# Kernel tuning notes

Hardware: AMD Instinct MI355X
Metric: run time of the kernel (lower is better)

## Reference

```python
import jax, jax.numpy as jnp
import numpy as np

N, E, B = 50000, 100000, 512   # nodes, edges, graphs
H, F_NODE, F_EDGE, T_OUT = 64, 16, 8, 1
T = 3                           # message-passing steps


def setup_inputs() -> dict:
    key = jax.random.key(0)
    ks = jax.random.split(key, 18)

    def w(k, shape, fan_in):
        return jax.random.normal(k, shape, dtype=jnp.float32) / np.sqrt(fan_in)

    return {
        "node_features": jax.random.normal(ks[0], (N, F_NODE), dtype=jnp.float32),
        "edge_features": jax.random.normal(ks[1], (E, F_EDGE), dtype=jnp.float32),
        "Esrc": jax.random.randint(ks[2], (E,), 0, N, dtype=jnp.int32),
        "Etgt": jax.random.randint(ks[3], (E,), 0, N, dtype=jnp.int32),
        "batch": jnp.sort(jax.random.randint(ks[4], (N,), 0, B, dtype=jnp.int32)),
        # input linear: node_features -> hidden
        "Win": w(ks[5], (H, F_NODE), F_NODE),
        "bin_": jnp.zeros((H,), jnp.float32),
        # edge encoder MLP: edge_features -> hidden -> hidden*hidden
        "We1": w(ks[6], (H, F_EDGE), F_EDGE),
        "be1": jnp.zeros((H,), jnp.float32),
        "We2": w(ks[7], (H * H, H), H),
        "be2": jnp.zeros((H * H,), jnp.float32),
        # GRU cell (shared across T steps)
        "Wih": w(ks[8], (3 * H, H), H),
        "bih": jnp.zeros((3 * H,), jnp.float32),
        "Whh": w(ks[9], (3 * H, H), H),
        "bhh": jnp.zeros((3 * H,), jnp.float32),
        # output linear: hidden -> target_features
        "Wout": w(ks[10], (T_OUT, H), H),
        "bout": jnp.zeros((T_OUT,), jnp.float32),
    }


def _gru(x, h, Wih, bih, Whh, bhh):
    gi = x @ Wih.T + bih            # [N, 3H]
    gh = h @ Whh.T + bhh
    i_r, i_z, i_n = jnp.split(gi, 3, axis=-1)
    h_r, h_z, h_n = jnp.split(gh, 3, axis=-1)
    r = jax.nn.sigmoid(i_r + h_r)
    z = jax.nn.sigmoid(i_z + h_z)
    n = jnp.tanh(i_n + r * h_n)
    return (1.0 - z) * n + z * h


def reference(node_features, edge_features, Esrc, Etgt, batch,
              Win, bin_, We1, be1, We2, be2,
              Wih, bih, Whh, bhh, Wout, bout):
    # Edge encoder MLP -> per-edge [H, H] message matrix (ENN style)
    eh = jax.nn.relu(edge_features @ We1.T + be1)          # [E, H]
    edge_data = (eh @ We2.T + be2).reshape(E, H, H)        # [E, H, H]

    x = node_features @ Win.T + bin_                       # [N, H]

    for _ in range(T):  # small fixed layer count
        msg = jnp.einsum('eij,ej->ei', edge_data, x[Esrc])  # per-edge matvec
        agg = jax.ops.segment_sum(msg, Etgt, num_segments=N)
        x = _gru(agg, x, Wih, bih, Whh, bhh)

    out = x @ Wout.T + bout                                # [N, 1]
    pooled = jax.ops.segment_sum(out, batch, num_segments=B)  # [B, 1]
    return pooled
```

## Files before the change

kernel.cpp:

```cpp
#include <hip/hip_runtime.h>
#include <hip/hip_fp16.h>

#define NN 50000
#define NE 100000
#define NB 512

typedef _Float16 f16x8 __attribute__((ext_vector_type(8)));
typedef float f32x4  __attribute__((ext_vector_type(4)));

__device__ __forceinline__ float sigm(float v) { return 1.0f / (1.0f + __expf(-v)); }
__device__ __forceinline__ float tanh_fast(float v) {
    float e = __expf(-2.0f * fabsf(v));
    float t = (1.0f - e) / (1.0f + e);
    return v < 0.f ? -t : t;
}

__global__ __launch_bounds__(256) void node_in_kernel(
    const float* __restrict__ nf, const float* __restrict__ Win,
    const float* __restrict__ bin_, float* __restrict__ x, __half* __restrict__ xh)
{
    int idx = blockIdx.x * 256 + threadIdx.x;
    if (idx >= NN * 64) return;
    int n = idx >> 6, h = idx & 63;
    float acc = bin_[h];
    #pragma unroll
    for (int f = 0; f < 16; f++) acc += nf[n * 16 + f] * Win[h * 16 + f];
    x[idx] = acc;
    xh[idx] = __float2half(acc);
}

__global__ __launch_bounds__(256) void edge_l1_kernel(
    const float* __restrict__ ef, const float* __restrict__ We1,
    const float* __restrict__ be1, __half* __restrict__ ehh)
{
    int idx = blockIdx.x * 256 + threadIdx.x;
    if (idx >= NE * 64) return;
    int e = idx >> 6, k = idx & 63;
    float acc = be1[k];
    #pragma unroll
    for (int f = 0; f < 8; f++) acc += ef[e * 8 + f] * We1[k * 8 + f];
    ehh[idx] = __float2half(fmaxf(acc, 0.0f));
}

__global__ __launch_bounds__(256) void pack_b_kernel(
    const float* __restrict__ We2, const float* __restrict__ be2,
    __half* __restrict__ Bp)
{
    int idx = blockIdx.x * 256 + threadIdx.x;
    if (idx >= 130 * 64 * 32) return;
    int kk = idx & 31;
    int n  = (idx >> 5) & 63;
    int kt = idx >> 11;
    int p  = kt * 32 + kk;
    float v;
    if (p < 4096) {
        int j = p >> 6, k = p & 63;
        v = We2[((size_t)(n * 64 + j)) * 64 + k];
    } else {
        v = be2[n * 64 + (p - 4096)];
    }
    Bp[idx] = __float2half(v);
}

__global__ __launch_bounds__(256) void pack_gru_kernel(
    const float* __restrict__ Wih, const float* __restrict__ Whh,
    __half* __restrict__ WG)
{
    int idx = blockIdx.x * 256 + threadIdx.x;
    if (idx >= 24576) return;
    int kk = idx & 31;
    int n  = (idx >> 5) & 15;
    int nt = (idx >> 9) % 24;
    int kt = (idx >> 9) / 24;
    int k = kt * 32 + kk;
    int col192 = (nt % 12) * 16 + n;
    int gate = col192 >> 6, h = col192 & 63;
    const float* src = (nt < 12) ? Wih : Whh;
    WG[idx] = __float2half(src[((size_t)(gate * 64 + h)) * 64 + k]);
}

__global__ __launch_bounds__(256, 3) void msg_kernel(
    const __half* __restrict__ xh, const __half* __restrict__ ehh,
    const __half* __restrict__ Bp,
    const int* __restrict__ Esrc, const int* __restrict__ Etgt,
    float* __restrict__ agg)
{
    __shared__ __half xs[4][64][72];
    __shared__ int tgt_s[256];
    const int tid = threadIdx.x;
    const int e0 = blockIdx.x * 256;
    const int w = tid >> 6, lane = tid & 63;

    {
        const int e = e0 + tid;
        const bool ok = (e < NE);
        const int src = ok ? Esrc[e] : 0;
        tgt_s[tid] = ok ? Etgt[e] : -1;
        const uint4* xsrc = (const uint4*)(xh + (size_t)src * 64);
        #pragma unroll
        for (int i = 0; i < 8; i++) {
            uint4 v = ok ? xsrc[i] : make_uint4(0, 0, 0, 0);
            *(uint4*)(&xs[w][lane][i * 8]) = v;
        }
    }
    __syncthreads();

    const int m = lane & 15;
    const int quad = lane >> 4;

    __half2 ehc2[4][2][4];
    #pragma unroll
    for (int mt = 0; mt < 4; mt++) {
        const int e = e0 + w * 64 + mt * 16 + m;
        if (e < NE) {
            union { uint4 u; __half2 h[4]; } u0, u1;
            u0.u = *(const uint4*)(ehh + (size_t)e * 64 + quad * 8);
            u1.u = *(const uint4*)(ehh + (size_t)e * 64 + 32 + quad * 8);
            #pragma unroll
            for (int q = 0; q < 4; q++) { ehc2[mt][0][q] = u0.h[q]; ehc2[mt][1][q] = u1.h[q]; }
        } else {
            __half2 z = __halves2half2(__float2half(0.f), __float2half(0.f));
            #pragma unroll
            for (int q = 0; q < 4; q++) { ehc2[mt][0][q] = z; ehc2[mt][1][q] = z; }
        }
    }

    f32x4 acc[4][4];
    #pragma unroll
    for (int a = 0; a < 4; a++)
        #pragma unroll
        for (int b = 0; b < 4; b++)
            #pragma unroll
            for (int q = 0; q < 4; q++) acc[a][b][q] = 0.f;

    const __half* blane = Bp + m * 32 + quad * 8;

    #pragma unroll 1
    for (int j = 0; j < 64; j++) {
        __half2 xsj2[4];
        #pragma unroll
        for (int mt = 0; mt < 4; mt++) {
            __half v = xs[w][mt * 16 + m][j];
            xsj2[mt] = __halves2half2(v, v);
        }
        #pragma unroll
        for (int half = 0; half < 2; half++) {
            const int kt = 2 * j + half;
            f16x8 bfrag[4];
            #pragma unroll
            for (int nt = 0; nt < 4; nt++)
                bfrag[nt] = *(const f16x8*)(blane + (size_t)kt * 2048 + nt * 512);
            #pragma unroll
            for (int mt = 0; mt < 4; mt++) {
                union { __half2 h[4]; f16x8 v; } u;
                #pragma unroll
                for (int q = 0; q < 4; q++)
                    u.h[q] = __hmul2(xsj2[mt], ehc2[mt][half][q]);
                #pragma unroll
                for (int nt = 0; nt < 4; nt++)
                    acc[mt][nt] = __builtin_amdgcn_mfma_f32_16x16x32_f16(
                        u.v, bfrag[nt], acc[mt][nt], 0, 0, 0);
            }
        }
    }

    #pragma unroll
    for (int half = 0; half < 2; half++) {
        const int kt = 128 + half;
        f16x8 bfrag[4];
        #pragma unroll
        for (int nt = 0; nt < 4; nt++)
            bfrag[nt] = *(const f16x8*)(blane + (size_t)kt * 2048 + nt * 512);
        #pragma unroll
        for (int mt = 0; mt < 4; mt++) {
            f16x8 af = *(const f16x8*)(&xs[w][mt * 16 + m][half * 32 + quad * 8]);
            #pragma unroll
            for (int nt = 0; nt < 4; nt++)
                acc[mt][nt] = __builtin_amdgcn_mfma_f32_16x16x32_f16(
                    af, bfrag[nt], acc[mt][nt], 0, 0, 0);
        }
    }

    #pragma unroll
    for (int mt = 0; mt < 4; mt++) {
        #pragma unroll
        for (int r = 0; r < 4; r++) {
            const int row = w * 64 + mt * 16 + quad * 4 + r;
            const int t = tgt_s[row];
            if (t >= 0) {
                #pragma unroll
                for (int nt = 0; nt < 4; nt++)
                    atomicAdd(agg + (size_t)t * 64 + nt * 16 + m, acc[mt][nt][r]);
            }
        }
    }
}

__global__ __launch_bounds__(256, 3) void gru_kernel(
    const float* __restrict__ agg, float* __restrict__ x, __half* __restrict__ xh,
    const __half* __restrict__ WG,
    const float* __restrict__ bih, const float* __restrict__ bhh)
{
    __shared__ __half wlds[24576];
    const int tid = threadIdx.x;
    {
        const uint4* src = (const uint4*)WG;
        uint4* dst = (uint4*)wlds;
        #pragma unroll
        for (int i = 0; i < 12; i++) dst[i * 256 + tid] = src[i * 256 + tid];
    }
    __syncthreads();

    const int w = tid >> 6, lane = tid & 63, m = lane & 15, quad = lane >> 4;
    const int nbase = blockIdx.x * 64 + w * 16;
    const int anode = nbase + m;
    const bool aok = (anode < NN);

    f16x8 a_agg[2], a_x[2];
    #pragma unroll
    for (int kt = 0; kt < 2; kt++) {
        const int koff = kt * 32 + quad * 8;
        if (aok) {
            const float* ap = agg + (size_t)anode * 64 + koff;
            float4 f0 = *(const float4*)ap;
            float4 f1 = *(const float4*)(ap + 4);
            union { __half2 h[4]; f16x8 v; } u;
            u.h[0] = __floats2half2_rn(f0.x, f0.y);
            u.h[1] = __floats2half2_rn(f0.z, f0.w);
            u.h[2] = __floats2half2_rn(f1.x, f1.y);
            u.h[3] = __floats2half2_rn(f1.z, f1.w);
            a_agg[kt] = u.v;
            a_x[kt] = *(const f16x8*)(xh + (size_t)anode * 64 + koff);
        } else {
            f16x8 z;
            #pragma unroll
            for (int i = 0; i < 8; i++) z[i] = (_Float16)0;
            a_agg[kt] = z; a_x[kt] = z;
        }
    }

    f32x4 acc[24];
    #pragma unroll
    for (int nt = 0; nt < 24; nt++)
        #pragma unroll
        for (int q = 0; q < 4; q++) acc[nt][q] = 0.f;

    #pragma unroll
    for (int kt = 0; kt < 2; kt++) {
        #pragma unroll
        for (int nt = 0; nt < 24; nt++) {
            f16x8 b = *(const f16x8*)(wlds + (kt * 24 + nt) * 512 + m * 32 + quad * 8);
            acc[nt] = __builtin_amdgcn_mfma_f32_16x16x32_f16(
                (nt < 12) ? a_agg[kt] : a_x[kt], b, acc[nt], 0, 0, 0);
        }
    }

    #pragma unroll
    for (int t = 0; t < 4; t++) {
        const int h = t * 16 + m;
        const float bir = bih[h], biz = bih[64 + h], bin = bih[128 + h];
        const float bhr = bhh[h], bhz = bhh[64 + h], bhn = bhh[128 + h];
        #pragma unroll
        for (int r = 0; r < 4; r++) {
            const int nd = nbase + quad * 4 + r;
            if (nd >= NN) continue;
            float ir  = acc[t][r]      + bir;
            float iz  = acc[4 + t][r]  + biz;
            float in_ = acc[8 + t][r]  + bin;
            float hr  = acc[12 + t][r] + bhr;
            float hz  = acc[16 + t][r] + bhz;
            float hn  = acc[20 + t][r] + bhn;
            float rg = sigm(ir + hr);
            float z  = sigm(iz + hz);
            float n  = tanh_fast(in_ + rg * hn);
            float xold = x[(size_t)nd * 64 + h];
            float xn = (1.0f - z) * n + z * xold;
            x[(size_t)nd * 64 + h] = xn;
            xh[(size_t)nd * 64 + h] = __float2half(xn);
        }
    }
}

__global__ __launch_bounds__(256) void pool_kernel(
    const float* __restrict__ x, const float* __restrict__ Wout,
    const float* __restrict__ bout, const int* __restrict__ batch,
    float* __restrict__ out)
{
    const int node = blockIdx.x * 256 + threadIdx.x;
    if (node >= NN) return;
    float acc = bout[0];
    const float4* xp = (const float4*)(x + (size_t)node * 64);
    #pragma unroll
    for (int i = 0; i < 16; i++) {
        float4 v = xp[i];
        acc += v.x * Wout[4*i] + v.y * Wout[4*i+1] + v.z * Wout[4*i+2] + v.w * Wout[4*i+3];
    }
    atomicAdd(out + batch[node], acc);
}

extern "C" void kernel_launch(void* const* d_in, const int* in_sizes, int n_in,
                              void* d_out, int out_size, void* d_ws, size_t ws_size,
                              hipStream_t stream)
{
    const float* nf   = (const float*)d_in[0];
    const float* ef   = (const float*)d_in[1];
    const int*   Esrc = (const int*)  d_in[2];
    const int*   Etgt = (const int*)  d_in[3];
    const int*   bat  = (const int*)  d_in[4];
    const float* Win  = (const float*)d_in[5];
    const float* bin_ = (const float*)d_in[6];
    const float* We1  = (const float*)d_in[7];
    const float* be1  = (const float*)d_in[8];
    const float* We2  = (const float*)d_in[9];
    const float* be2  = (const float*)d_in[10];
    const float* Wih  = (const float*)d_in[11];
    const float* bih  = (const float*)d_in[12];
    const float* Whh  = (const float*)d_in[13];
    const float* bhh  = (const float*)d_in[14];
    const float* Wout = (const float*)d_in[15];
    const float* bout = (const float*)d_in[16];

    char* ws = (char*)d_ws;
    float*  x   = (float*)(ws);
    float*  agg = (float*)(ws + 12800000);
    __half* xh  = (__half*)(ws + 25600000);
    __half* ehh = (__half*)(ws + 32000000);
    __half* Bp  = (__half*)(ws + 44800000);
    __half* WG  = (__half*)(ws + 45400064);

    hipMemsetAsync(d_out, 0, NB * sizeof(float), stream);

    node_in_kernel<<<(NN * 64 + 255) / 256, 256, 0, stream>>>(nf, Win, bin_, x, xh);
    edge_l1_kernel<<<(NE * 64 + 255) / 256, 256, 0, stream>>>(ef, We1, be1, ehh);
    pack_b_kernel<<<(130 * 64 * 32 + 255) / 256, 256, 0, stream>>>(We2, be2, Bp);
    pack_gru_kernel<<<(24576 + 255) / 256, 256, 0, stream>>>(Wih, Whh, WG);

    for (int t = 0; t < 3; t++) {
        hipMemsetAsync(agg, 0, (size_t)NN * 64 * sizeof(float), stream);
        msg_kernel<<<(NE + 255) / 256, 256, 0, stream>>>(xh, ehh, Bp, Esrc, Etgt, agg);
        gru_kernel<<<(NN + 63) / 64, 256, 0, stream>>>(agg, x, xh, WG, bih, bhh);
    }

    pool_kernel<<<(NN + 255) / 256, 256, 0, stream>>>(x, Wout, bout, bat, (float*)d_out);
}
```

Baseline: 476.8 us.

## Stage edge-weight B tiles in LDS and switch message kernel to 32x32 MFMA

The message kernel now stages chunks of the packed We2 matrix into shared memory, loaded cooperatively by the block, instead of having each lane read B fragments from global memory. It switches from 16x16x32 to 32x32x16 MFMA tiles, with a new B packing layout to match. The aim is to cut repeated global or L2 traffic for the shared weight matrix and to issue fewer, larger MFMAs. Separately, the GRU kernel becomes a persistent grid-stride loop over 512 blocks so the GRU weights are loaded into LDS fewer times, and hipMemsetAsync is replaced by a custom zero-fill kernel. The price is extra __syncthreads per chunk, more LDS per block, and a lower occupancy target for the message kernel.

```diff
diff --git a/kernel.cpp b/kernel.cpp
--- a/kernel.cpp
+++ b/kernel.cpp
@@ -6,7 +6,9 @@
 #define NB 512
 
 typedef _Float16 f16x8 __attribute__((ext_vector_type(8)));
+typedef _Float16 f16x4 __attribute__((ext_vector_type(4)));
 typedef float f32x4  __attribute__((ext_vector_type(4)));
+typedef float f32x16 __attribute__((ext_vector_type(16)));
 
 __device__ __forceinline__ float sigm(float v) { return 1.0f / (1.0f + __expf(-v)); }
 __device__ __forceinline__ float tanh_fast(float v) {
@@ -15,6 +17,13 @@
     return v < 0.f ? -t : t;
 }
 
+__global__ void fill0_kernel(float4* __restrict__ p, int n4)
+{
+    int i = blockIdx.x * 256 + threadIdx.x;
+    const int stride = gridDim.x * 256;
+    for (; i < n4; i += stride) p[i] = make_float4(0.f, 0.f, 0.f, 0.f);
+}
+
 __global__ __launch_bounds__(256) void node_in_kernel(
     const float* __restrict__ nf, const float* __restrict__ Win,
     const float* __restrict__ bin_, float* __restrict__ x, __half* __restrict__ xh)
@@ -42,22 +51,25 @@
     ehh[idx] = __float2half(fmaxf(acc, 0.0f));
 }
 
-__global__ __launch_bounds__(256) void pack_b_kernel(
+__global__ __launch_bounds__(256) void pack_b32_kernel(
     const float* __restrict__ We2, const float* __restrict__ be2,
     __half* __restrict__ Bp)
 {
     int idx = blockIdx.x * 256 + threadIdx.x;
-    if (idx >= 130 * 64 * 32) return;
-    int kk = idx & 31;
-    int n  = (idx >> 5) & 63;
-    int kt = idx >> 11;
-    int p  = kt * 32 + kk;
+    if (idx >= 260 * 1024) return;
+    int i  = idx & 7;
+    int n  = (idx >> 3) & 31;
+    int hi = (idx >> 8) & 1;
+    int nt = (idx >> 9) & 1;
+    int kt = idx >> 10;
+    int p  = kt * 16 + hi * 8 + i;
+    int col = nt * 32 + n;
     float v;
     if (p < 4096) {
         int j = p >> 6, k = p & 63;
-        v = We2[((size_t)(n * 64 + j)) * 64 + k];
+        v = We2[((size_t)(col * 64 + j)) * 64 + k];
     } else {
-        v = be2[n * 64 + (p - 4096)];
+        v = be2[col * 64 + (p - 4096)];
     }
     Bp[idx] = __float2half(v);
 }
@@ -79,17 +91,19 @@
     WG[idx] = __float2half(src[((size_t)(gate * 64 + h)) * 64 + k]);
 }
 
-__global__ __launch_bounds__(256, 3) void msg_kernel(
+__global__ __launch_bounds__(256, 2) void msg_kernel(
     const __half* __restrict__ xh, const __half* __restrict__ ehh,
     const __half* __restrict__ Bp,
     const int* __restrict__ Esrc, const int* __restrict__ Etgt,
     float* __restrict__ agg)
 {
-    __shared__ __half xs[4][64][72];
+    __shared__ __attribute__((aligned(16))) __half xs[256 * 72];
+    __shared__ __attribute__((aligned(16))) __half bst[16 * 1024];
     __shared__ int tgt_s[256];
     const int tid = threadIdx.x;
     const int e0 = blockIdx.x * 256;
     const int w = tid >> 6, lane = tid & 63;
+    const int n32 = lane & 31, hi = lane >> 5;
 
     {
         const int e = e0 + tid;
@@ -100,97 +114,100 @@
         #pragma unroll
         for (int i = 0; i < 8; i++) {
             uint4 v = ok ? xsrc[i] : make_uint4(0, 0, 0, 0);
-            *(uint4*)(&xs[w][lane][i * 8]) = v;
-        }
-    }
-    __syncthreads();
-
-    const int m = lane & 15;
-    const int quad = lane >> 4;
-
-    __half2 ehc2[4][2][4];
-    #pragma unroll
-    for (int mt = 0; mt < 4; mt++) {
-        const int e = e0 + w * 64 + mt * 16 + m;
+            *(uint4*)(&xs[tid * 72 + i * 8]) = v;
+        }
+    }
+
+    __half2 ehc[2][4][4];
+    #pragma unroll
+    for (int mt = 0; mt < 2; mt++) {
+        const int e = e0 + w * 64 + mt * 32 + n32;
         if (e < NE) {
-            union { uint4 u; __half2 h[4]; } u0, u1;
-            u0.u = *(const uint4*)(ehh + (size_t)e * 64 + quad * 8);
-            u1.u = *(const uint4*)(ehh + (size_t)e * 64 + 32 + quad * 8);
-            #pragma unroll
-            for (int q = 0; q < 4; q++) { ehc2[mt][0][q] = u0.h[q]; ehc2[mt][1][q] = u1.h[q]; }
+            #pragma unroll
+            for (int c4 = 0; c4 < 4; c4++) {
+                union { uint4 u; __half2 h[4]; } u;
+                u.u = *(const uint4*)(ehh + (size_t)e * 64 + c4 * 16 + hi * 8);
+                #pragma unroll
+                for (int q = 0; q < 4; q++) ehc[mt][c4][q] = u.h[q];
+            }
         } else {
-            __half2 z = __halves2half2(__float2half(0.f), __float2half(0.f));
-            #pragma unroll
-            for (int q = 0; q < 4; q++) { ehc2[mt][0][q] = z; ehc2[mt][1][q] = z; }
-        }
-    }
-
-    f32x4 acc[4][4];
-    #pragma unroll
-    for (int a = 0; a < 4; a++)
-        #pragma unroll
-        for (int b = 0; b < 4; b++)
-            #pragma unroll
-            for (int q = 0; q < 4; q++) acc[a][b][q] = 0.f;
-
-    const __half* blane = Bp + m * 32 + quad * 8;
+            __half2 z = __half2half2(__float2half(0.f));
+            #pragma unroll
+            for (int c4 = 0; c4 < 4; c4++)
+                #pragma unroll
+                for (int q = 0; q < 4; q++) ehc[mt][c4][q] = z;
+        }
+    }
+
+    f32x16 acc[2][2];
+    #pragma unroll
+    for (int a = 0; a < 2; a++)
+        #pragma unroll
+        for (int b = 0; b < 2; b++)
+            #pragma unroll
+            for (int q = 0; q < 16; q++) acc[a][b][q] = 0.f;
+
+    const int rowA0 = w * 64 + n32;
+    const __half* blane = bst + hi * 256 + n32 * 8;
 
     #pragma unroll 1
-    for (int j = 0; j < 64; j++) {
-        __half2 xsj2[4];
-        #pragma unroll
-        for (int mt = 0; mt < 4; mt++) {
-            __half v = xs[w][mt * 16 + m][j];
-            xsj2[mt] = __halves2half2(v, v);
-        }
-        #pragma unroll
-        for (int half = 0; half < 2; half++) {
-            const int kt = 2 * j + half;
-            f16x8 bfrag[4];
-            #pragma unroll
-            for (int nt = 0; nt < 4; nt++)
-                bfrag[nt] = *(const f16x8*)(blane + (size_t)kt * 2048 + nt * 512);
-            #pragma unroll
-            for (int mt = 0; mt < 4; mt++) {
-                union { __half2 h[4]; f16x8 v; } u;
-                #pragma unroll
-                for (int q = 0; q < 4; q++)
-                    u.h[q] = __hmul2(xsj2[mt], ehc2[mt][half][q]);
-                #pragma unroll
-                for (int nt = 0; nt < 4; nt++)
-                    acc[mt][nt] = __builtin_amdgcn_mfma_f32_16x16x32_f16(
-                        u.v, bfrag[nt], acc[mt][nt], 0, 0, 0);
-            }
-        }
-    }
-
-    #pragma unroll
-    for (int half = 0; half < 2; half++) {
-        const int kt = 128 + half;
-        f16x8 bfrag[4];
-        #pragma unroll
-        for (int nt = 0; nt < 4; nt++)
-            bfrag[nt] = *(const f16x8*)(blane + (size_t)kt * 2048 + nt * 512);
-        #pragma unroll
-        for (int mt = 0; mt < 4; mt++) {
-            f16x8 af = *(const f16x8*)(&xs[w][mt * 16 + m][half * 32 + quad * 8]);
-            #pragma unroll
-            for (int nt = 0; nt < 4; nt++)
-                acc[mt][nt] = __builtin_amdgcn_mfma_f32_16x16x32_f16(
-                    af, bfrag[nt], acc[mt][nt], 0, 0, 0);
-        }
-    }
-
-    #pragma unroll
-    for (int mt = 0; mt < 4; mt++) {
-        #pragma unroll
-        for (int r = 0; r < 4; r++) {
-            const int row = w * 64 + mt * 16 + quad * 4 + r;
-            const int t = tgt_s[row];
+    for (int c = 0; c < 17; c++) {
+        const int nkt = (c < 16) ? 16 : 4;
+        __syncthreads();
+        {
+            const __half* gsrc = Bp + (size_t)c * 16384;
+            for (int i = 0; i < nkt / 2; i++)
+                *(uint4*)(bst + (size_t)(i * 256 + tid) * 8) =
+                    *(const uint4*)(gsrc + (size_t)(i * 256 + tid) * 8);
+        }
+        __syncthreads();
+
+        if (c < 16) {
+            f16x4 xr4[2];
+            #pragma unroll
+            for (int mt = 0; mt < 2; mt++)
+                xr4[mt] = *(const f16x4*)(xs + (rowA0 + mt * 32) * 72 + c * 4);
+            #pragma unroll
+            for (int u = 0; u < 16; u++) {
+                f16x8 b0 = *(const f16x8*)(blane + u * 1024);
+                f16x8 b1 = *(const f16x8*)(blane + u * 1024 + 512);
+                const int c4 = u & 3;
+                const int jq = u >> 2;
+                #pragma unroll
+                for (int mt = 0; mt < 2; mt++) {
+                    union { f16x4 v; __half h[4]; } xu; xu.v = xr4[mt];
+                    __half2 xv2 = __half2half2(xu.h[jq]);
+                    union { __half2 h[4]; f16x8 v; } a;
+                    #pragma unroll
+                    for (int q = 0; q < 4; q++) a.h[q] = __hmul2(xv2, ehc[mt][c4][q]);
+                    acc[mt][0] = __builtin_amdgcn_mfma_f32_32x32x16_f16(a.v, b0, acc[mt][0], 0, 0, 0);
+                    acc[mt][1] = __builtin_amdgcn_mfma_f32_32x32x16_f16(a.v, b1, acc[mt][1], 0, 0, 0);
+                }
+            }
+        } else {
+            #pragma unroll
+            for (int u = 0; u < 4; u++) {
+                f16x8 b0 = *(const f16x8*)(blane + u * 1024);
+                f16x8 b1 = *(const f16x8*)(blane + u * 1024 + 512);
+                #pragma unroll
+                for (int mt = 0; mt < 2; mt++) {
+                    f16x8 a = *(const f16x8*)(xs + (rowA0 + mt * 32) * 72 + u * 16 + hi * 8);
+                    acc[mt][0] = __builtin_amdgcn_mfma_f32_32x32x16_f16(a, b0, acc[mt][0], 0, 0, 0);
+                    acc[mt][1] = __builtin_amdgcn_mfma_f32_32x32x16_f16(a, b1, acc[mt][1], 0, 0, 0);
+                }
+            }
+        }
+    }
+
+    #pragma unroll
+    for (int mt = 0; mt < 2; mt++) {
+        #pragma unroll
+        for (int r = 0; r < 16; r++) {
+            const int rowe = (r & 3) + 8 * (r >> 2) + 4 * hi;
+            const int t = tgt_s[w * 64 + mt * 32 + rowe];
             if (t >= 0) {
-                #pragma unroll
-                for (int nt = 0; nt < 4; nt++)
-                    atomicAdd(agg + (size_t)t * 64 + nt * 16 + m, acc[mt][nt][r]);
+                atomicAdd(agg + (size_t)t * 64 + n32, acc[mt][0][r]);
+                atomicAdd(agg + (size_t)t * 64 + 32 + n32, acc[mt][1][r]);
             }
         }
     }
@@ -201,7 +218,7 @@
     const __half* __restrict__ WG,
     const float* __restrict__ bih, const float* __restrict__ bhh)
 {
-    __shared__ __half wlds[24576];
+    __shared__ __attribute__((aligned(16))) __half wlds[24576];
     const int tid = threadIdx.x;
     {
         const uint4* src = (const uint4*)WG;
@@ -212,71 +229,75 @@
     __syncthreads();
 
     const int w = tid >> 6, lane = tid & 63, m = lane & 15, quad = lane >> 4;
-    const int nbase = blockIdx.x * 64 + w * 16;
-    const int anode = nbase + m;
-    const bool aok = (anode < NN);
-
-    f16x8 a_agg[2], a_x[2];
-    #pragma unroll
-    for (int kt = 0; kt < 2; kt++) {
-        const int koff = kt * 32 + quad * 8;
-        if (aok) {
-            const float* ap = agg + (size_t)anode * 64 + koff;
-            float4 f0 = *(const float4*)ap;
-            float4 f1 = *(const float4*)(ap + 4);
-            union { __half2 h[4]; f16x8 v; } u;
-            u.h[0] = __floats2half2_rn(f0.x, f0.y);
-            u.h[1] = __floats2half2_rn(f0.z, f0.w);
-            u.h[2] = __floats2half2_rn(f1.x, f1.y);
-            u.h[3] = __floats2half2_rn(f1.z, f1.w);
-            a_agg[kt] = u.v;
-            a_x[kt] = *(const f16x8*)(xh + (size_t)anode * 64 + koff);
-        } else {
-            f16x8 z;
-            #pragma unroll
-            for (int i = 0; i < 8; i++) z[i] = (_Float16)0;
-            a_agg[kt] = z; a_x[kt] = z;
-        }
-    }
-
-    f32x4 acc[24];
-    #pragma unroll
-    for (int nt = 0; nt < 24; nt++)
-        #pragma unroll
-        for (int q = 0; q < 4; q++) acc[nt][q] = 0.f;
-
-    #pragma unroll
-    for (int kt = 0; kt < 2; kt++) {
-        #pragma unroll
-        for (int nt = 0; nt < 24; nt++) {
-            f16x8 b = *(const f16x8*)(wlds + (kt * 24 + nt) * 512 + m * 32 + quad * 8);
-            acc[nt] = __builtin_amdgcn_mfma_f32_16x16x32_f16(
-                (nt < 12) ? a_agg[kt] : a_x[kt], b, acc[nt], 0, 0, 0);
-        }
-    }
-
-    #pragma unroll
-    for (int t = 0; t < 4; t++) {
-        const int h = t * 16 + m;
-        const float bir = bih[h], biz = bih[64 + h], bin = bih[128 + h];
-        const float bhr = bhh[h], bhz = bhh[64 + h], bhn = bhh[128 + h];
-        #pragma unroll
-        for (int r = 0; r < 4; r++) {
-            const int nd = nbase + quad * 4 + r;
-            if (nd >= NN) continue;
-            float ir  = acc[t][r]      + bir;
-            float iz  = acc[4 + t][r]  + biz;
-            float in_ = acc[8 + t][r]  + bin;
-            float hr  = acc[12 + t][r] + bhr;
-            float hz  = acc[16 + t][r] + bhz;
-            float hn  = acc[20 + t][r] + bhn;
-            float rg = sigm(ir + hr);
-            float z  = sigm(iz + hz);
-            float n  = tanh_fast(in_ + rg * hn);
-            float xold = x[(size_t)nd * 64 + h];
-            float xn = (1.0f - z) * n + z * xold;
-            x[(size_t)nd * 64 + h] = xn;
-            xh[(size_t)nd * 64 + h] = __float2half(xn);
+
+    #pragma unroll 1
+    for (int tile = blockIdx.x; tile < (NN + 63) / 64; tile += 512) {
+        const int nbase = tile * 64 + w * 16;
+        const int anode = nbase + m;
+        const bool aok = (anode < NN);
+
+        f16x8 a_agg[2], a_x[2];
+        #pragma unroll
+        for (int kt = 0; kt < 2; kt++) {
+            const int koff = kt * 32 + quad * 8;
+            if (aok) {
+                const float* ap = agg + (size_t)anode * 64 + koff;
+                float4 f0 = *(const float4*)ap;
+                float4 f1 = *(const float4*)(ap + 4);
+                union { __half2 h[4]; f16x8 v; } u;
+                u.h[0] = __floats2half2_rn(f0.x, f0.y);
+                u.h[1] = __floats2half2_rn(f0.z, f0.w);
+                u.h[2] = __floats2half2_rn(f1.x, f1.y);
+                u.h[3] = __floats2half2_rn(f1.z, f1.w);
+                a_agg[kt] = u.v;
+                a_x[kt] = *(const f16x8*)(xh + (size_t)anode * 64 + koff);
+            } else {
+                f16x8 z;
+                #pragma unroll
+                for (int i = 0; i < 8; i++) z[i] = (_Float16)0;
+                a_agg[kt] = z; a_x[kt] = z;
+            }
+        }
+
+        f32x4 acc[24];
+        #pragma unroll
+        for (int nt = 0; nt < 24; nt++)
+            #pragma unroll
+            for (int q = 0; q < 4; q++) acc[nt][q] = 0.f;
+
+        #pragma unroll
+        for (int kt = 0; kt < 2; kt++) {
+            #pragma unroll
+            for (int nt = 0; nt < 24; nt++) {
+                f16x8 b = *(const f16x8*)(wlds + (kt * 24 + nt) * 512 + m * 32 + quad * 8);
+                acc[nt] = __builtin_amdgcn_mfma_f32_16x16x32_f16(
+                    (nt < 12) ? a_agg[kt] : a_x[kt], b, acc[nt], 0, 0, 0);
+            }
+        }
+
+        #pragma unroll
+        for (int t = 0; t < 4; t++) {
+            const int h = t * 16 + m;
+            const float bir = bih[h], biz = bih[64 + h], bin = bih[128 + h];
+            const float bhr = bhh[h], bhz = bhh[64 + h], bhn = bhh[128 + h];
+            #pragma unroll
+            for (int r = 0; r < 4; r++) {
+                const int nd = nbase + quad * 4 + r;
+                if (nd >= NN) continue;
+                float ir  = acc[t][r]      + bir;
+                float iz  = acc[4 + t][r]  + biz;
+                float in_ = acc[8 + t][r]  + bin;
+                float hr  = acc[12 + t][r] + bhr;
+                float hz  = acc[16 + t][r] + bhz;
+                float hn  = acc[20 + t][r] + bhn;
+                float rg = sigm(ir + hr);
+                float z  = sigm(iz + hz);
+                float n  = tanh_fast(in_ + rg * hn);
+                float xold = x[(size_t)nd * 64 + h];
+                float xn = (1.0f - z) * n + z * xold;
+                x[(size_t)nd * 64 + h] = xn;
+                xh[(size_t)nd * 64 + h] = __float2half(xn);
+            }
         }
     }
 }
@@ -332,13 +353,13 @@
 
     node_in_kernel<<<(NN * 64 + 255) / 256, 256, 0, stream>>>(nf, Win, bin_, x, xh);
     edge_l1_kernel<<<(NE * 64 + 255) / 256, 256, 0, stream>>>(ef, We1, be1, ehh);
-    pack_b_kernel<<<(130 * 64 * 32 + 255) / 256, 256, 0, stream>>>(We2, be2, Bp);
+    pack_b32_kernel<<<(260 * 1024 + 255) / 256, 256, 0, stream>>>(We2, be2, Bp);
     pack_gru_kernel<<<(24576 + 255) / 256, 256, 0, stream>>>(Wih, Whh, WG);
 
     for (int t = 0; t < 3; t++) {
-        hipMemsetAsync(agg, 0, (size_t)NN * 64 * sizeof(float), stream);
+        fill0_kernel<<<1024, 256, 0, stream>>>((float4*)agg, NN * 16);
         msg_kernel<<<(NE + 255) / 256, 256, 0, stream>>>(xh, ehh, Bp, Esrc, Etgt, agg);
-        gru_kernel<<<(NN + 63) / 64, 256, 0, stream>>>(agg, x, xh, WG, bih, bhh);
+        gru_kernel<<<512, 256, 0, stream>>>(agg, x, xh, WG, bih, bhh);
     }
 
     pool_kernel<<<(NN + 255) / 256, 256, 0, stream>>>(x, Wout, bout, bat, (float*)d_out);
```

After: 551.0 us. 1.16x slower.
